# Kernel optimization log

Hardware: AMD Instinct MI355X
Metric: run time of the kernel (lower is better)

## Reference

```python
import jax, jax.numpy as jnp
import numpy as np

EPS = 1e-5

def ter_quant(w):
    # BitNet b1.58 absmean ternary quantization: scale by mean(|W|), round to {-1,0,1}, rescale.
    gamma = jnp.mean(jnp.abs(w)) + EPS
    wq = jnp.clip(jnp.round(w / gamma), -1.0, 1.0) * gamma
    return wq

def setup_inputs() -> dict:
    key = jax.random.key(0)
    k_x, k_w1, k_w2 = jax.random.split(key, 3)
    B, S, D, H = 64, 197, 768, 3072
    x = jax.random.normal(k_x, (B, S, D), dtype=jnp.float32)
    w1 = jax.random.normal(k_w1, (H, D), dtype=jnp.float32) * (1.0 / np.sqrt(D))
    b1 = jnp.zeros((H,), dtype=jnp.float32)
    w2 = jax.random.normal(k_w2, (D, H), dtype=jnp.float32) * (1.0 / np.sqrt(H))
    b2 = jnp.zeros((D,), dtype=jnp.float32)
    return {"x": x, "w1": w1, "b1": b1, "w2": w2, "b2": b2}

def reference(x, w1, b1, w2, b2):
    # fc1: ternary-quantized linear, exact GELU, fc2: ternary-quantized linear (dropout p=0 is identity)
    h = jnp.einsum('bsd,hd->bsh', x, ter_quant(w1)) + b1
    h = jax.nn.gelu(h, approximate=False)
    y = jnp.einsum('bsh,dh->bsd', h, ter_quant(w2)) + b2
    return y
```

## Files before the change

### kernel.cpp

```cpp
#include <hip/hip_runtime.h>
#include <hip/hip_bf16.h>
#include <math.h>

typedef __bf16 bf16_t;
typedef __bf16 bf16x8 __attribute__((ext_vector_type(8)));
typedef __bf16 bf16x4 __attribute__((ext_vector_type(4)));
typedef float f32x4 __attribute__((ext_vector_type(4)));

#define QEPS 1e-5

__device__ __forceinline__ void gload_lds16(const void* g, void* l) {
  __builtin_amdgcn_global_load_lds((const __attribute__((address_space(1))) void*)g,
                                   (__attribute__((address_space(3))) void*)l, 16, 0, 0);
}

__device__ __forceinline__ float gelu_exact(float x) {
  float a = x * 0.7071067811865476f;
  float s = fabsf(a);
  float t = __builtin_amdgcn_rcpf(__builtin_fmaf(0.3275911f, s, 1.0f));
  float p = __builtin_fmaf(1.061405429f, t, -1.453152027f);
  p = __builtin_fmaf(p, t, 1.421413741f);
  p = __builtin_fmaf(p, t, -0.284496736f);
  p = __builtin_fmaf(p, t, 0.254829592f);
  p = p * t;
  float e = __expf(-s * s);
  float er = copysignf(__builtin_fmaf(-p, e, 1.0f), a);
  return 0.5f * x * (1.0f + er);
}

__global__ void reduce_abs2_kernel(const float* __restrict__ w1, const float* __restrict__ w2,
                                   int n, double* __restrict__ out) {
  const int nb = gridDim.x >> 1;
  const bool second = blockIdx.x >= nb;
  const float* __restrict__ w = second ? w2 : w1;
  const int b = second ? blockIdx.x - nb : blockIdx.x;
  double s = 0.0;
  const int stride = nb * blockDim.x * 4;
  for (int i = (b * blockDim.x + threadIdx.x) * 4; i < n; i += stride) {
    float4 v = *(const float4*)(w + i);
    s += (double)fabsf(v.x) + (double)fabsf(v.y) + (double)fabsf(v.z) + (double)fabsf(v.w);
  }
  for (int off = 32; off > 0; off >>= 1)
    s += __shfl_down(s, off, 64);
  __shared__ double ls[4];
  int lane = threadIdx.x & 63, wv = threadIdx.x >> 6;
  if (lane == 0) ls[wv] = s;
  __syncthreads();
  if (threadIdx.x == 0)
    atomicAdd(out + (second ? 1 : 0), ls[0] + ls[1] + ls[2] + ls[3]);
}

__global__ void quantize2_kernel(const float* __restrict__ w1, const float* __restrict__ w2,
                                 int n, const double* __restrict__ sums, double cnt,
                                 bf16_t* __restrict__ q1, bf16_t* __restrict__ q2) {
  int i4 = blockIdx.x * blockDim.x + threadIdx.x;
  const int half4 = n >> 2;
  const float* w;
  bf16_t* q;
  double g;
  int idx;
  if (i4 < half4) { w = w1; q = q1; g = sums[0]; idx = i4; }
  else            { w = w2; q = q2; g = sums[1]; idx = i4 - half4; }
  g = g / cnt + QEPS;
  float4 v = ((const float4*)w)[idx];
  bf16x4 r;
  {
    double t0 = fmin(1.0, fmax(-1.0, rint((double)v.x / g)));
    double t1 = fmin(1.0, fmax(-1.0, rint((double)v.y / g)));
    double t2 = fmin(1.0, fmax(-1.0, rint((double)v.z / g)));
    double t3 = fmin(1.0, fmax(-1.0, rint((double)v.w / g)));
    r[0] = (bf16_t)(float)t0; r[1] = (bf16_t)(float)t1;
    r[2] = (bf16_t)(float)t2; r[3] = (bf16_t)(float)t3;
  }
  ((bf16x4*)q)[idx] = r;
}

__global__ void cast_pad_kernel(const float* __restrict__ x, bf16_t* __restrict__ xb,
                                long long nvalid, long long ntotal) {
  long long i = ((long long)blockIdx.x * blockDim.x + threadIdx.x) * 4;
  if (i >= ntotal) return;
  bf16x4 r;
  if (i < nvalid) {
    float4 v = *(const float4*)(x + i);
    r[0] = (bf16_t)v.x; r[1] = (bf16_t)v.y; r[2] = (bf16_t)v.z; r[3] = (bf16_t)v.w;
  } else {
    r[0] = (bf16_t)0.0f; r[1] = (bf16_t)0.0f; r[2] = (bf16_t)0.0f; r[3] = (bf16_t)0.0f;
  }
  *(bf16x4*)(xb + i) = r;
}

template <int EPI>
__global__ __launch_bounds__(256, 4)
void gemm_bt_kernel(const bf16_t* __restrict__ A, const bf16_t* __restrict__ B,
                    const float* __restrict__ bias,
                    const double* __restrict__ sumptr, double cnt,
                    void* __restrict__ Cout, int N, int K, int Mvalid, int gx) {
  __shared__ bf16_t sA[128 * 64];
  __shared__ bf16_t sB[128 * 64];

  const int G = gridDim.x;
  const int f = blockIdx.x;
  const int xcd = f & 7;
  const int idx = f >> 3;
  const int q8 = G >> 3, r8 = G & 7;
  const int t = xcd * q8 + (xcd < r8 ? xcd : r8) + idx;
  const int bx = t % gx;
  const int by = t / gx;

  const int tid = threadIdx.x;
  const int lane = tid & 63;
  const int wave = tid >> 6;
  const int wr = (wave >> 1) * 64;
  const int wc = (wave & 1) * 64;
  const int row16 = lane & 15;
  const int quad = lane >> 4;

  const size_t Ks = (size_t)K;
  const int slot = tid & 7;
  const int cg = slot ^ ((tid >> 3) & 7);
  const bf16_t* gA = A + ((size_t)(by * 128 + (tid >> 3))) * Ks + (size_t)cg * 8;
  const bf16_t* gB = B + ((size_t)(bx * 128 + (tid >> 3))) * Ks + (size_t)cg * 8;
  bf16_t* lA = sA + wave * 512;
  bf16_t* lB = sB + wave * 512;

  f32x4 acc[4][4] = {};

  for (int k0 = 0; k0 < K; k0 += 64) {
#pragma unroll
    for (int n = 0; n < 4; n++) {
      gload_lds16(gA + (size_t)(n * 32) * Ks, lA + n * 2048);
      gload_lds16(gB + (size_t)(n * 32) * Ks, lB + n * 2048);
    }
    gA += 64;
    gB += 64;
    __syncthreads();

#pragma unroll
    for (int kk = 0; kk < 2; kk++) {
      bf16x8 afr[4], bfr[4];
      const int swz = ((kk * 4 + quad) ^ (row16 & 7)) * 8;
#pragma unroll
      for (int i = 0; i < 4; i++)
        afr[i] = *(const bf16x8*)&sA[(wr + i * 16 + row16) * 64 + swz];
#pragma unroll
      for (int j = 0; j < 4; j++)
        bfr[j] = *(const bf16x8*)&sB[(wc + j * 16 + row16) * 64 + swz];
#pragma unroll
      for (int i = 0; i < 4; i++)
#pragma unroll
        for (int j = 0; j < 4; j++)
          acc[i][j] = __builtin_amdgcn_mfma_f32_16x16x32_bf16(afr[i], bfr[j], acc[i][j], 0, 0, 0);
    }
    __syncthreads();
  }

  const float gamma = (float)(sumptr[0] / cnt + QEPS);
  const int c_base = bx * 128 + wc + row16;
  const int r_base = by * 128 + wr + quad * 4;

  if constexpr (EPI == 0) {
    bf16_t* sE = sA;
    float bv[4];
#pragma unroll
    for (int j = 0; j < 4; j++) bv[j] = bias[c_base + j * 16];
    bf16_t* h = (bf16_t*)Cout;
#pragma unroll
    for (int i = 0; i < 4; i++) {
#pragma unroll
      for (int j = 0; j < 4; j++) {
        const int col = wc + j * 16 + row16;
#pragma unroll
        for (int r = 0; r < 4; r++) {
          const int e = (wave >> 1) * 16 + quad * 4 + r;
          float v = gelu_exact(gamma * acc[i][j][r] + bv[j]);
          sE[e * 136 + col] = (bf16_t)v;
        }
      }
      __syncthreads();
      {
        const int e = tid >> 3, ch = tid & 7;
        const int grow = by * 128 + (e >> 4) * 64 + i * 16 + (e & 15);
        bf16_t* dst = &h[(size_t)grow * N + bx * 128];
        *(bf16x8*)&dst[ch * 8] = *(const bf16x8*)&sE[e * 136 + ch * 8];
        *(bf16x8*)&dst[ch * 8 + 64] = *(const bf16x8*)&sE[e * 136 + ch * 8 + 64];
      }
      __syncthreads();
    }
  } else {
    float* out = (float*)Cout;
#pragma unroll
    for (int j = 0; j < 4; j++) {
      const int col = c_base + j * 16;
      const float bv = bias[col];
#pragma unroll
      for (int i = 0; i < 4; i++) {
#pragma unroll
        for (int r = 0; r < 4; r++) {
          const int row = r_base + i * 16 + r;
          if (row < Mvalid)
            out[(size_t)row * N + col] = gamma * acc[i][j][r] + bv;
        }
      }
    }
  }
}

extern "C" void kernel_launch(void* const* d_in, const int* in_sizes, int n_in,
                              void* d_out, int out_size, void* d_ws, size_t ws_size,
                              hipStream_t stream) {
  const float* x  = (const float*)d_in[0];
  const float* w1 = (const float*)d_in[1];
  const float* b1 = (const float*)d_in[2];
  const float* w2 = (const float*)d_in[3];
  const float* b2 = (const float*)d_in[4];
  float* out = (float*)d_out;

  const int M = 64 * 197;
  const int Mpad = 12672;
  const int D = 768, H = 3072;
  const int nW = H * D;

  char* ws = (char*)d_ws;
  double* sums = (double*)ws;
  bf16_t* xb  = (bf16_t*)(ws + 256);
  bf16_t* w1q = xb + (size_t)Mpad * D;
  bf16_t* w2q = w1q + (size_t)H * D;
  bf16_t* hb  = w2q + (size_t)D * H;

  hipMemsetAsync(sums, 0, 2 * sizeof(double), stream);
  reduce_abs2_kernel<<<512, 256, 0, stream>>>(w1, w2, nW, sums);
  quantize2_kernel<<<(2 * nW / 4) / 256, 256, 0, stream>>>(w1, w2, nW, sums, (double)nW, w1q, w2q);
  cast_pad_kernel<<<((long long)Mpad * D / 4) / 256, 256, 0, stream>>>(
      x, xb, (long long)M * D, (long long)Mpad * D);

  const int gy = Mpad / 128;
  const int gx1 = H / 128;
  const int gx2 = D / 128;
  gemm_bt_kernel<0><<<gx1 * gy, 256, 0, stream>>>(xb, w1q, b1, sums + 0, (double)nW, hb, H, D, M, gx1);
  gemm_bt_kernel<1><<<gx2 * gy, 256, 0, stream>>>(hb, w2q, b2, sums + 1, (double)nW, out, D, H, M, gx2);
}
```

Before: 262.7 us.

## Fuse quantize and cast prep kernels, drop memset, use 64-wide N tile for fc2

The atomic reduction and memset become per-block partial sums. The partials are reduced redundantly inside a merged prep kernel that also quantizes both weights and casts/pads x in one launch, removing two launches and a memset. The fc2 GEMM now uses a 128x64 tile, giving twice as many blocks (12 column tiles instead of 6) to improve occupancy across CUs for the narrow N=768 output. The cost is less B-operand reuse per block and redundant partial-sum reduction in every quantize block.

```diff
diff --git a/kernel.cpp b/kernel.cpp
--- a/kernel.cpp
+++ b/kernel.cpp
@@ -28,15 +28,14 @@
   return 0.5f * x * (1.0f + er);
 }
 
-__global__ void reduce_abs2_kernel(const float* __restrict__ w1, const float* __restrict__ w2,
-                                   int n, double* __restrict__ out) {
-  const int nb = gridDim.x >> 1;
-  const bool second = blockIdx.x >= nb;
+__global__ void reduce_part_kernel(const float* __restrict__ w1, const float* __restrict__ w2,
+                                   int n, double* __restrict__ part) {
+  const bool second = blockIdx.x >= 256;
   const float* __restrict__ w = second ? w2 : w1;
-  const int b = second ? blockIdx.x - nb : blockIdx.x;
+  const int b = second ? blockIdx.x - 256 : blockIdx.x;
   double s = 0.0;
-  const int stride = nb * blockDim.x * 4;
-  for (int i = (b * blockDim.x + threadIdx.x) * 4; i < n; i += stride) {
+  const int stride = 256 * 256 * 4;
+  for (int i = (b * 256 + threadIdx.x) * 4; i < n; i += stride) {
     float4 v = *(const float4*)(w + i);
     s += (double)fabsf(v.x) + (double)fabsf(v.y) + (double)fabsf(v.z) + (double)fabsf(v.w);
   }
@@ -46,57 +45,57 @@
   int lane = threadIdx.x & 63, wv = threadIdx.x >> 6;
   if (lane == 0) ls[wv] = s;
   __syncthreads();
-  if (threadIdx.x == 0)
-    atomicAdd(out + (second ? 1 : 0), ls[0] + ls[1] + ls[2] + ls[3]);
-}
-
-__global__ void quantize2_kernel(const float* __restrict__ w1, const float* __restrict__ w2,
-                                 int n, const double* __restrict__ sums, double cnt,
-                                 bf16_t* __restrict__ q1, bf16_t* __restrict__ q2) {
-  int i4 = blockIdx.x * blockDim.x + threadIdx.x;
-  const int half4 = n >> 2;
-  const float* w;
-  bf16_t* q;
-  double g;
-  int idx;
-  if (i4 < half4) { w = w1; q = q1; g = sums[0]; idx = i4; }
-  else            { w = w2; q = q2; g = sums[1]; idx = i4 - half4; }
-  g = g / cnt + QEPS;
-  float4 v = ((const float4*)w)[idx];
-  bf16x4 r;
-  {
-    double t0 = fmin(1.0, fmax(-1.0, rint((double)v.x / g)));
-    double t1 = fmin(1.0, fmax(-1.0, rint((double)v.y / g)));
-    double t2 = fmin(1.0, fmax(-1.0, rint((double)v.z / g)));
-    double t3 = fmin(1.0, fmax(-1.0, rint((double)v.w / g)));
-    r[0] = (bf16_t)(float)t0; r[1] = (bf16_t)(float)t1;
-    r[2] = (bf16_t)(float)t2; r[3] = (bf16_t)(float)t3;
-  }
-  ((bf16x4*)q)[idx] = r;
-}
-
-__global__ void cast_pad_kernel(const float* __restrict__ x, bf16_t* __restrict__ xb,
-                                long long nvalid, long long ntotal) {
-  long long i = ((long long)blockIdx.x * blockDim.x + threadIdx.x) * 4;
-  if (i >= ntotal) return;
-  bf16x4 r;
-  if (i < nvalid) {
-    float4 v = *(const float4*)(x + i);
-    r[0] = (bf16_t)v.x; r[1] = (bf16_t)v.y; r[2] = (bf16_t)v.z; r[3] = (bf16_t)v.w;
+  if (threadIdx.x == 0) part[blockIdx.x] = ls[0] + ls[1] + ls[2] + ls[3];
+}
+
+__global__ void prep_kernel(const float* __restrict__ w1, const float* __restrict__ w2,
+                            const float* __restrict__ x, const double* __restrict__ part,
+                            int nW, long long nxv, bf16_t* __restrict__ q1,
+                            bf16_t* __restrict__ q2, bf16_t* __restrict__ xb,
+                            double* __restrict__ gammas) {
+  const int QB = (nW >> 1) >> 8;
+  const int tid = threadIdx.x;
+  if (blockIdx.x < QB) {
+    const int half = QB >> 1;
+    const bool second = blockIdx.x >= half;
+    double p = part[(second ? 256 : 0) + tid];
+    for (int off = 32; off > 0; off >>= 1)
+      p += __shfl_down(p, off, 64);
+    __shared__ double red[4];
+    if ((tid & 63) == 0) red[tid >> 6] = p;
+    __syncthreads();
+    const double g = (red[0] + red[1] + red[2] + red[3]) / (double)nW + QEPS;
+    if (tid == 0 && blockIdx.x == (second ? half : 0)) gammas[second ? 1 : 0] = g;
+    const double rg = 1.0 / g;
+    const int idx = blockIdx.x * 256 + tid - (second ? (nW >> 2) : 0);
+    const float4 v = ((const float4*)(second ? w2 : w1))[idx];
+    bf16x4 r;
+    r[0] = (bf16_t)(float)fmin(1.0, fmax(-1.0, rint((double)v.x * rg)));
+    r[1] = (bf16_t)(float)fmin(1.0, fmax(-1.0, rint((double)v.y * rg)));
+    r[2] = (bf16_t)(float)fmin(1.0, fmax(-1.0, rint((double)v.z * rg)));
+    r[3] = (bf16_t)(float)fmin(1.0, fmax(-1.0, rint((double)v.w * rg)));
+    ((bf16x4*)(second ? q2 : q1))[idx] = r;
   } else {
-    r[0] = (bf16_t)0.0f; r[1] = (bf16_t)0.0f; r[2] = (bf16_t)0.0f; r[3] = (bf16_t)0.0f;
-  }
-  *(bf16x4*)(xb + i) = r;
-}
-
-template <int EPI>
+    long long i = ((long long)(blockIdx.x - QB) * 256 + tid) * 4;
+    bf16x4 r;
+    if (i < nxv) {
+      float4 v = *(const float4*)(x + i);
+      r[0] = (bf16_t)v.x; r[1] = (bf16_t)v.y; r[2] = (bf16_t)v.z; r[3] = (bf16_t)v.w;
+    } else {
+      r[0] = (bf16_t)0.0f; r[1] = (bf16_t)0.0f; r[2] = (bf16_t)0.0f; r[3] = (bf16_t)0.0f;
+    }
+    *(bf16x4*)(xb + i) = r;
+  }
+}
+
+template <int EPI, int BN>
 __global__ __launch_bounds__(256, 4)
 void gemm_bt_kernel(const bf16_t* __restrict__ A, const bf16_t* __restrict__ B,
-                    const float* __restrict__ bias,
-                    const double* __restrict__ sumptr, double cnt,
+                    const float* __restrict__ bias, const double* __restrict__ gptr,
                     void* __restrict__ Cout, int N, int K, int Mvalid, int gx) {
+  constexpr int NJ = BN / 32;
   __shared__ bf16_t sA[128 * 64];
-  __shared__ bf16_t sB[128 * 64];
+  __shared__ bf16_t sB[BN * 64];
 
   const int G = gridDim.x;
   const int f = blockIdx.x;
@@ -111,63 +110,63 @@
   const int lane = tid & 63;
   const int wave = tid >> 6;
   const int wr = (wave >> 1) * 64;
-  const int wc = (wave & 1) * 64;
+  const int wc = (wave & 1) * (BN / 2);
   const int row16 = lane & 15;
   const int quad = lane >> 4;
 
   const size_t Ks = (size_t)K;
-  const int slot = tid & 7;
-  const int cg = slot ^ ((tid >> 3) & 7);
+  const int cg = (tid & 7) ^ ((tid >> 3) & 7);
   const bf16_t* gA = A + ((size_t)(by * 128 + (tid >> 3))) * Ks + (size_t)cg * 8;
-  const bf16_t* gB = B + ((size_t)(bx * 128 + (tid >> 3))) * Ks + (size_t)cg * 8;
+  const bf16_t* gB = B + ((size_t)(bx * BN + (tid >> 3))) * Ks + (size_t)cg * 8;
   bf16_t* lA = sA + wave * 512;
   bf16_t* lB = sB + wave * 512;
 
-  f32x4 acc[4][4] = {};
+  f32x4 acc[4][NJ] = {};
 
   for (int k0 = 0; k0 < K; k0 += 64) {
 #pragma unroll
-    for (int n = 0; n < 4; n++) {
+    for (int n = 0; n < 4; n++)
       gload_lds16(gA + (size_t)(n * 32) * Ks, lA + n * 2048);
+#pragma unroll
+    for (int n = 0; n < BN / 32; n++)
       gload_lds16(gB + (size_t)(n * 32) * Ks, lB + n * 2048);
-    }
     gA += 64;
     gB += 64;
     __syncthreads();
 
 #pragma unroll
     for (int kk = 0; kk < 2; kk++) {
-      bf16x8 afr[4], bfr[4];
+      bf16x8 afr[4], bfr[NJ];
       const int swz = ((kk * 4 + quad) ^ (row16 & 7)) * 8;
 #pragma unroll
       for (int i = 0; i < 4; i++)
         afr[i] = *(const bf16x8*)&sA[(wr + i * 16 + row16) * 64 + swz];
 #pragma unroll
-      for (int j = 0; j < 4; j++)
+      for (int j = 0; j < NJ; j++)
         bfr[j] = *(const bf16x8*)&sB[(wc + j * 16 + row16) * 64 + swz];
 #pragma unroll
       for (int i = 0; i < 4; i++)
 #pragma unroll
-        for (int j = 0; j < 4; j++)
+        for (int j = 0; j < NJ; j++)
           acc[i][j] = __builtin_amdgcn_mfma_f32_16x16x32_bf16(afr[i], bfr[j], acc[i][j], 0, 0, 0);
     }
     __syncthreads();
   }
 
-  const float gamma = (float)(sumptr[0] / cnt + QEPS);
-  const int c_base = bx * 128 + wc + row16;
+  const float gamma = (float)gptr[0];
+  const int c_base = bx * BN + wc + row16;
   const int r_base = by * 128 + wr + quad * 4;
 
   if constexpr (EPI == 0) {
     bf16_t* sE = sA;
-    float bv[4];
-#pragma unroll
-    for (int j = 0; j < 4; j++) bv[j] = bias[c_base + j * 16];
+    float bv[NJ];
+#pragma unroll
+    for (int j = 0; j < NJ; j++) bv[j] = bias[c_base + j * 16];
     bf16_t* h = (bf16_t*)Cout;
 #pragma unroll
     for (int i = 0; i < 4; i++) {
 #pragma unroll
-      for (int j = 0; j < 4; j++) {
+      for (int j = 0; j < NJ; j++) {
         const int col = wc + j * 16 + row16;
 #pragma unroll
         for (int r = 0; r < 4; r++) {
@@ -180,7 +179,7 @@
       {
         const int e = tid >> 3, ch = tid & 7;
         const int grow = by * 128 + (e >> 4) * 64 + i * 16 + (e & 15);
-        bf16_t* dst = &h[(size_t)grow * N + bx * 128];
+        bf16_t* dst = &h[(size_t)grow * N + bx * BN];
         *(bf16x8*)&dst[ch * 8] = *(const bf16x8*)&sE[e * 136 + ch * 8];
         *(bf16x8*)&dst[ch * 8 + 64] = *(const bf16x8*)&sE[e * 136 + ch * 8 + 64];
       }
@@ -189,7 +188,7 @@
   } else {
     float* out = (float*)Cout;
 #pragma unroll
-    for (int j = 0; j < 4; j++) {
+    for (int j = 0; j < NJ; j++) {
       const int col = c_base + j * 16;
       const float bv = bias[col];
 #pragma unroll
@@ -221,21 +220,22 @@
   const int nW = H * D;
 
   char* ws = (char*)d_ws;
-  double* sums = (double*)ws;
-  bf16_t* xb  = (bf16_t*)(ws + 256);
+  double* part = (double*)ws;
+  double* gammas = (double*)(ws + 4096);
+  bf16_t* xb  = (bf16_t*)(ws + 4096 + 256);
   bf16_t* w1q = xb + (size_t)Mpad * D;
   bf16_t* w2q = w1q + (size_t)H * D;
   bf16_t* hb  = w2q + (size_t)D * H;
 
-  hipMemsetAsync(sums, 0, 2 * sizeof(double), stream);
-  reduce_abs2_kernel<<<512, 256, 0, stream>>>(w1, w2, nW, sums);
-  quantize2_kernel<<<(2 * nW / 4) / 256, 256, 0, stream>>>(w1, w2, nW, sums, (double)nW, w1q, w2q);
-  cast_pad_kernel<<<((long long)Mpad * D / 4) / 256, 256, 0, stream>>>(
-      x, xb, (long long)M * D, (long long)Mpad * D);
+  reduce_part_kernel<<<512, 256, 0, stream>>>(w1, w2, nW, part);
+  const int QB = (nW >> 1) >> 8;
+  const int CB = (int)(((long long)Mpad * D / 4) / 256);
+  prep_kernel<<<QB + CB, 256, 0, stream>>>(w1, w2, x, part, nW, (long long)M * D,
+                                           w1q, w2q, xb, gammas);
 
   const int gy = Mpad / 128;
   const int gx1 = H / 128;
-  const int gx2 = D / 128;
-  gemm_bt_kernel<0><<<gx1 * gy, 256, 0, stream>>>(xb, w1q, b1, sums + 0, (double)nW, hb, H, D, M, gx1);
-  gemm_bt_kernel<1><<<gx2 * gy, 256, 0, stream>>>(hb, w2q, b2, sums + 1, (double)nW, out, D, H, M, gx2);
-}
+  const int gx2 = D / 64;
+  gemm_bt_kernel<0, 128><<<gx1 * gy, 256, 0, stream>>>(xb, w1q, b1, gammas + 0, hb, H, D, M, gx1);
+  gemm_bt_kernel<1, 64><<<gx2 * gy, 256, 0, stream>>>(hb, w2q, b2, gammas + 1, out, D, H, M, gx2);
+}
```

Result: no change. 258.4 us (-1.6%).
